# Kernel tuning notes

Measured on AMD Instinct MI355X. Metric: run time of the kernel, lower is better.

The kernel has to match this reference:

```python
import jax, jax.numpy as jnp
import numpy as np
from jax import lax

B, N = 1, 16384
HID = 128
ITERS = 32           # sphere_tracing_iters
SECANT_ITERS = 8     # root-finding refinement steps
THR = 1e-5           # root_finding_threshold
CLAMP = 0.1          # clamp_dist for sphere tracing steps
SN, SF = 16, 16      # near/far surface sample counts
SVR = 0.05           # surface_vol_range (meters)


def setup_inputs():
    key = jax.random.key(0)
    ks = jax.random.split(key, 10)
    cam_loc = jax.random.normal(ks[0], (B, 3)) * 0.1 + jnp.array([0.0, 0.0, 3.0])
    d = jax.random.normal(ks[1], (B, N, 3)) * 0.3 + jnp.array([0.0, 0.0, -1.0])
    ray_directions = d / jnp.linalg.norm(d, axis=-1, keepdims=True)
    near = 1.0 + 0.5 * jax.random.uniform(ks[2], (B, N))
    far = near + 1.0 + jax.random.uniform(ks[3], (B, N))
    body_bounds_intersections = jnp.stack([near, far], axis=-1)
    smpl_verts = jax.random.normal(ks[4], (B, 6890, 3)) * 0.5
    smpl_verts_cano = jax.random.normal(ks[5], (B, 6890, 3)) * 0.5
    sw = jax.random.uniform(ks[6], (B, 6890, 24))
    skinning_weights = sw / jnp.sum(sw, axis=-1, keepdims=True)
    bone_transforms = jnp.broadcast_to(jnp.eye(4), (B, 24, 4, 4)).copy()
    loc = jnp.zeros((B, 1, 3)); sc_factor = jnp.ones((B, 1, 3)); trans = jnp.zeros((B, 1, 3))
    coord_min = -1.2 * jnp.ones((B, 1, 3)); coord_max = 1.2 * jnp.ones((B, 1, 3)); center = jnp.zeros((B, 1, 3))
    W1 = jax.random.normal(ks[7], (3, HID)) / np.sqrt(3.0)
    W2 = jax.random.normal(ks[8], (HID, HID)) / np.sqrt(HID)
    W3 = jax.random.normal(ks[9], (HID, 1)) / np.sqrt(HID)
    b1 = jnp.zeros((HID,)); b2 = jnp.zeros((HID,)); b3 = jnp.zeros((1,))
    return dict(cam_loc=cam_loc, ray_directions=ray_directions,
                body_bounds_intersections=body_bounds_intersections, loc=loc,
                sc_factor=sc_factor, smpl_verts=smpl_verts, smpl_verts_cano=smpl_verts_cano,
                skinning_weights=skinning_weights, bone_transforms=bone_transforms, trans=trans,
                coord_min=coord_min, coord_max=coord_max, center=center,
                W1=W1, b1=b1, W2=W2, b2=b2, W3=W3, b3=b3)


def _forward(cam_loc, ray_directions, body_bounds_intersections, loc, sc_factor,
             smpl_verts, smpl_verts_cano, skinning_weights, bone_transforms, trans,
             coord_min, coord_max, center, W1, b1, W2, b2, W3, b3):
    cam = cam_loc[:, None, :]                       # [B,1,3]
    dirs = ray_directions                            # [B,N,3]
    near = body_bounds_intersections[..., 0]         # [B,N]
    far = body_bounds_intersections[..., 1]

    def to_cano(x):  # world -> normalized canonical coords
        x = (x - trans - loc) * sc_factor
        return (x - center) / ((coord_max - coord_min) * 0.5)

    def sdf_mlp(xn):
        h = jax.nn.softplus(xn @ W1 + b1)
        h = jax.nn.softplus(h @ W2 + b2)
        return (h @ W3 + b3)[..., 0]

    def sdf_at(t):  # t: [B,N] -> (sdf [B,N], pts_norm [B,N,3])
        xn = to_cano(cam + t[..., None] * dirs)
        return sdf_mlp(xn), xn

    # ---- sphere tracing (fixed ITERS, mask-based early exit) ----
    unf0 = near < far
    div0 = ~unf0
    pts0 = to_cano(cam + near[..., None] * dirs)

    def st_step(carry, _):
        acc, unf, div, pts = carry
        s, xn = sdf_at(acc)
        conv = unf
        pts = jnp.where(conv[..., None], xn, pts)
        sm = jnp.clip(s, -CLAMP, CLAMP)
        upd = unf & (jnp.abs(sm) > THR) & (jnp.abs(s) < 1e6)
        acc = jnp.where(upd, acc + sm, acc)
        div = jnp.where(upd, acc >= far, div)
        remove = (conv & (jnp.abs(s) <= THR)) | div
        unf = unf & ~remove
        return (acc, unf, div, pts), None

    (acc, unf, div, pts), _ = lax.scan(st_step, (near, unf0, div0, pts0), None, length=ITERS)

    # ---- secant root finding on ray depth ----
    t0 = jnp.clip(acc - CLAMP, near, far)
    t1 = jnp.clip(acc, near, far)
    f0, _ = sdf_at(t0)

    def sec_step(carry, _):
        t0, f0, t1 = carry
        f1, _ = sdf_at(t1)
        denom = f0 - f1
        denom = jnp.where(jnp.abs(denom) < 1e-9, 1e-9, denom)
        t2 = jnp.clip(t1 - f1 * (t1 - t0) / denom, near, far)
        return (t1, f1, t2), None

    (t0, f0, t1), _ = lax.scan(sec_step, (t0, f0, t1), None, length=SECANT_ITERS)
    f1, xn1 = sdf_at(t1)
    conv_opt = (jnp.abs(f1) <= THR) & (t1 >= near) & (t1 <= far)

    curr_start_points = xn1                                    # [B,N,3] normalized
    acc_start_dis = jnp.where(conv_opt, t1, near)              # [B,N]
    network_body_mask = conv_opt

    # per-ray forward transforms: LBS with mean skinning weights (skinning net surrogate)
    w_mean = jnp.mean(skinning_weights, axis=1)
    w_mean = w_mean / jnp.sum(w_mean, axis=-1, keepdims=True)  # [B,24]
    T = jnp.einsum('bj,bjkl->bkl', w_mean, bone_transforms)    # [B,4,4]
    S = SN + SF
    sampler_transforms = jnp.broadcast_to(T[:, None, None], (T.shape[0], t1.shape[1], S, 4, 4))

    # ---- ray sampler (eval mode: no perturbation) ----
    u_n = jnp.linspace(0.0, 1.0, SN)
    z_near = (t1 - SVR)[..., None] + u_n * (2.0 * SVR)         # [B,N,SN]
    u_f = jnp.linspace(0.0, 1.0, SF)
    z_far = near[..., None] + u_f * (far - near)[..., None]    # [B,N,SF]
    z_surf = jnp.sort(jnp.concatenate([z_near, z_far], axis=-1), axis=-1)
    u_a = jnp.linspace(0.0, 1.0, S)
    z_uni = near[..., None] + u_a * (far - near)[..., None]
    z = jnp.where(conv_opt[..., None], z_surf, z_uni)          # [B,N,S]
    sampler_pts = to_cano(cam[:, :, None, :] + z[..., None] * dirs[:, :, None, :])
    sampler_dists = z
    sampler_converge_mask = conv_opt

    return (curr_start_points, network_body_mask, acc_start_dis,
            sampler_pts, sampler_dists, sampler_transforms, sampler_converge_mask)


def reference(cam_loc, ray_directions, body_bounds_intersections, loc, sc_factor,
              smpl_verts, smpl_verts_cano, skinning_weights, bone_transforms, trans,
              coord_min, coord_max, center, W1, b1, W2, b2, W3, b3):
    return _forward(cam_loc, ray_directions, body_bounds_intersections, loc, sc_factor,
                    smpl_verts, smpl_verts_cano, skinning_weights, bone_transforms, trans,
                    coord_min, coord_max, center, W1, b1, W2, b2, W3, b3)
```

## Files before the change

kernel.cpp:

```cpp
#include <hip/hip_runtime.h>

typedef short sh8 __attribute__((ext_vector_type(8)));
typedef __bf16 bf8 __attribute__((ext_vector_type(8)));
typedef float f4 __attribute__((ext_vector_type(4)));
typedef unsigned int u4 __attribute__((ext_vector_type(4)));

#define DEV __device__ __forceinline__

DEV unsigned int fbits(float f){ union{float f;unsigned int u;}v; v.f=f; return v.u; }
DEV float bitsf(unsigned int u){ union{unsigned int u;float f;}v; v.u=u; return v.f; }
DEV float bf2f(unsigned short u) { return bitsf(((unsigned int)u) << 16); }
DEV unsigned short f2bf(float f) {
    unsigned int x = fbits(f);
    return (unsigned short)((x + 0x7fffu + ((x >> 16) & 1u)) >> 16);
}
DEV float sp_f(float x) {
    float ax = fabsf(x);
    float e  = exp2f(ax * -1.4426950408889634f);
    float u  = 1.0f + e;
    float c  = e - (u - 1.0f);
    float lg = log2f(u);
    return fmaxf(x, 0.0f) + fmaf(0.69314718055994531f, lg, c * (2.0f - u));
}

#define MFMA(a, b, c) __builtin_amdgcn_mfma_f32_16x16x32_bf16(__builtin_bit_cast(bf8, a), __builtin_bit_cast(bf8, b), c, 0, 0, 0)

__global__ void t_kernel(const float* __restrict__ sw,
                         const float* __restrict__ bt,
                         float* __restrict__ Tout, int V) {
    __shared__ float red[4 * 24];
    __shared__ float mm[24];
    float p[24];
#pragma unroll
    for (int j = 0; j < 24; j++) p[j] = 0.0f;
    for (int v = threadIdx.x; v < V; v += 256) {
        const float* row = sw + v * 24;
#pragma unroll
        for (int c4 = 0; c4 < 6; c4++) {
            f4 a = *(const f4*)(row + c4 * 4);
#pragma unroll
            for (int e = 0; e < 4; e++) p[c4 * 4 + e] += a[e];
        }
    }
#pragma unroll
    for (int j = 0; j < 24; j++) {
#pragma unroll
        for (int msk = 1; msk < 64; msk <<= 1) p[j] += __shfl_xor(p[j], msk);
    }
    int lane = threadIdx.x & 63, wid = threadIdx.x >> 6;
    if (lane == 0) {
#pragma unroll
        for (int j = 0; j < 24; j++) red[wid * 24 + j] = p[j];
    }
    __syncthreads();
    if (threadIdx.x < 24) {
        float s = red[threadIdx.x] + red[24 + threadIdx.x] + red[48 + threadIdx.x] + red[72 + threadIdx.x];
        mm[threadIdx.x] = s / (float)V;
    }
    __syncthreads();
    if (threadIdx.x < 16) {
        float tot = 0.0f;
#pragma unroll
        for (int j = 0; j < 24; j++) tot += mm[j];
        float a = 0.0f;
#pragma unroll
        for (int j = 0; j < 24; j++) a += (mm[j] / tot) * bt[j * 16 + threadIdx.x];
        Tout[threadIdx.x] = a;
    }
}

__global__ __launch_bounds__(256, 1) void main_kernel(
    const float* __restrict__ cam_loc, const float* __restrict__ dirs,
    const float* __restrict__ bbi,     const float* __restrict__ loc,
    const float* __restrict__ scf,     const float* __restrict__ trans,
    const float* __restrict__ cmin,    const float* __restrict__ cmax,
    const float* __restrict__ cent,    const float* __restrict__ W1,
    const float* __restrict__ b1,      const float* __restrict__ W2,
    const float* __restrict__ b2,      const float* __restrict__ W3,
    const float* __restrict__ b3,      const float* __restrict__ Tmat,
    float* __restrict__ out, int N) {

    __shared__ unsigned short wfrag[3 * 16384];
    __shared__ f4 w1p[16 * 9];
    __shared__ float b2s[128], w3s[128];

    const int tid = threadIdx.x;

    for (int i4 = tid; i4 < 4096; i4 += 256) {
        f4 v = *(const f4*)(W2 + i4 * 4);
        int k = (i4 * 4) >> 7;
        int n0 = (i4 * 4) & 127;
        int lanehalf = ((k >> 3) & 3) << 4;
        int fk = k >> 5;
        int j = k & 7;
#pragma unroll
        for (int e = 0; e < 4; e++) {
            int n = n0 + e;
            float w = v[e];
            unsigned short u0 = f2bf(w);   float g0 = bf2f(u0);
            float r1 = w - g0;             unsigned short u1 = f2bf(r1); float g1 = bf2f(u1);
            float r2 = r1 - g1;            unsigned short u2 = f2bf(r2);
            int off = ((n >> 4) * 4 + fk) * 512 + (lanehalf | (n & 15)) * 8 + j;
            wfrag[off]         = u0;
            wfrag[16384 + off] = u1;
            wfrag[32768 + off] = u2;
        }
    }
    if (tid < 128) {
        int k = tid, ks = k >> 5, uu = (k >> 3) & 3, j = k & 7;
        f4 w;
        w.x = W1[k]; w.y = W1[128 + k]; w.z = W1[256 + k]; w.w = b1[k];
        w1p[(ks * 4 + uu) * 9 + j] = w;
        b2s[k] = b2[k];
        w3s[k] = W3[k];
    }
    __syncthreads();

    const int lane = tid & 63;
    const int wv = tid >> 6;
    const int m = lane & 15, u = lane >> 4;
    const int rayBase = (blockIdx.x * 4 + wv) * 16;
    const int R = rayBase + m;

    const int O1 = 3 * N, O2 = 4 * N, O3 = 5 * N, O4 = 101 * N, O5 = 133 * N, O6 = 645 * N;

    float camx = cam_loc[0], camy = cam_loc[1], camz = cam_loc[2];
    float A[3], Bc[3];
#pragma unroll
    for (int c = 0; c < 3; c++) {
        float he = 0.5f * (cmax[c] - cmin[c]);
        float sc = scf[c];
        float off = (0.0f - trans[c] - loc[c]) * sc - cent[c];
        A[c] = sc / he; Bc[c] = off / he;
    }
    float dx = dirs[R * 3 + 0], dy = dirs[R * 3 + 1], dz = dirs[R * 3 + 2];
    float nearv = bbi[R * 2 + 0], farv = bbi[R * 2 + 1];

    float w3v[8], b2v[8];
#pragma unroll
    for (int nt = 0; nt < 8; nt++) { w3v[nt] = w3s[nt * 16 + m]; b2v[nt] = b2s[nt * 16 + m]; }
    float b3v = b3[0];

    const int lane16 = lane * 8;

    auto EVAL = [&](float t, float& sout) {
        float y0 = fmaf(t, dx, camx), y1 = fmaf(t, dy, camy), y2 = fmaf(t, dz, camz);
        float x0 = fmaf(y0, A[0], Bc[0]), x1 = fmaf(y1, A[1], Bc[1]), x2 = fmaf(y2, A[2], Bc[2]);
        f4 c[8];
#pragma unroll
        for (int f = 0; f < 8; f++) {
            float b = b2v[f];
            c[f] = (f4){b, b, b, b};
        }
#pragma unroll 1
        for (int ks = 0; ks < 4; ks++) {
            u4 a0w, a1w, a2w;
#pragma unroll
            for (int jp = 0; jp < 4; jp++) {
                f4 wA = w1p[(ks * 4 + u) * 9 + 2 * jp];
                f4 wB = w1p[(ks * 4 + u) * 9 + 2 * jp + 1];
                float hA = fmaf(x0, wA.x, fmaf(x1, wA.y, fmaf(x2, wA.z, wA.w)));
                float hB = fmaf(x0, wB.x, fmaf(x1, wB.y, fmaf(x2, wB.z, wB.w)));
                float sA = sp_f(hA), sB = sp_f(hB);
                unsigned short A0 = f2bf(sA); float fA0 = bf2f(A0);
                unsigned short B0 = f2bf(sB); float fB0 = bf2f(B0);
                float rA1 = sA - fA0, rB1 = sB - fB0;
                unsigned short A1 = f2bf(rA1); float fA1 = bf2f(A1);
                unsigned short B1 = f2bf(rB1); float fB1 = bf2f(B1);
                float rA2 = rA1 - fA1, rB2 = rB1 - fB1;
                unsigned short A2 = f2bf(rA2);
                unsigned short B2 = f2bf(rB2);
                a0w[jp] = (unsigned int)A0 | ((unsigned int)B0 << 16);
                a1w[jp] = (unsigned int)A1 | ((unsigned int)B1 << 16);
                a2w[jp] = (unsigned int)A2 | ((unsigned int)B2 << 16);
            }
            const int base = ks * 512 + lane16;
#pragma unroll
            for (int f = 0; f < 8; f++) {
                int fi = f * 2048 + base;
                sh8 b0 = *(const sh8*)&wfrag[fi];
                sh8 b1f = *(const sh8*)&wfrag[16384 + fi];
                sh8 b2f = *(const sh8*)&wfrag[32768 + fi];
                c[f] = MFMA(a0w, b0, c[f]);
                c[f] = MFMA(a1w, b0, c[f]);
                c[f] = MFMA(a2w, b0, c[f]);
                c[f] = MFMA(a0w, b1f, c[f]);
                c[f] = MFMA(a1w, b1f, c[f]);
                c[f] = MFMA(a0w, b2f, c[f]);
            }
        }
        float pr0 = 0.f, pr1 = 0.f, pr2 = 0.f, pr3 = 0.f;
#pragma unroll
        for (int f = 0; f < 8; f++) {
            float wv3 = w3v[f];
            pr0 = fmaf(sp_f(c[f].x), wv3, pr0);
            pr1 = fmaf(sp_f(c[f].y), wv3, pr1);
            pr2 = fmaf(sp_f(c[f].z), wv3, pr2);
            pr3 = fmaf(sp_f(c[f].w), wv3, pr3);
        }
#pragma unroll
        for (int msk = 1; msk < 16; msk <<= 1) {
            pr0 += __shfl_xor(pr0, msk); pr1 += __shfl_xor(pr1, msk);
            pr2 += __shfl_xor(pr2, msk); pr3 += __shfl_xor(pr3, msk);
        }
        pr0 += b3v; pr1 += b3v; pr2 += b3v; pr3 += b3v;
        int srcl = (m >> 2) << 4;
        float q0 = __shfl(pr0, srcl), q1 = __shfl(pr1, srcl);
        float q2 = __shfl(pr2, srcl), q3 = __shfl(pr3, srcl);
        float sa = (m & 1) ? q1 : q0, sb = (m & 1) ? q3 : q2;
        sout = (m & 2) ? sb : sa;
    };

    float acc = nearv;
    bool unf = nearv < farv;
    bool dv = !unf;
    float sv;
#pragma unroll 1
    for (int it = 0; it < 32; ++it) {
        if (!__any((int)unf)) break;
        EVAL(acc, sv);
        float smv = fminf(fmaxf(sv, -0.1f), 0.1f);
        bool convu = unf;
        bool upd = unf && (fabsf(smv) > 1e-5f) && (fabsf(sv) < 1000000.0f);
        if (upd) acc = acc + smv;
        dv = upd ? (acc >= farv) : dv;
        bool remove = (convu && (fabsf(sv) <= 1e-5f)) || dv;
        unf = unf && !remove;
    }

    float t0 = fminf(fmaxf(acc - 0.1f, nearv), farv);
    float t1 = fminf(fmaxf(acc, nearv), farv);
    float f0;
    EVAL(t0, f0);
    float f1 = 0.0f;
#pragma unroll 1
    for (int si = 0; si < 9; ++si) {
        float f1s;
        EVAL(t1, f1s);
        if (si == 8) { f1 = f1s; break; }
        float den = f0 - f1s;
        den = (fabsf(den) < 1e-9f) ? 1e-9f : den;
        float t2 = t1 - f1s * (t1 - t0) / den;
        t2 = fminf(fmaxf(t2, nearv), farv);
        t0 = t1; f0 = f1s; t1 = t2;
    }
    bool conv = (fabsf(f1) <= 1e-5f) && (t1 >= nearv) && (t1 <= farv);

    float xv0, xv1, xv2;
    {
        float y0 = fmaf(t1, dx, camx), y1 = fmaf(t1, dy, camy), y2 = fmaf(t1, dz, camz);
        xv0 = fmaf(y0, A[0], Bc[0]); xv1 = fmaf(y1, A[1], Bc[1]); xv2 = fmaf(y2, A[2], Bc[2]);
    }

    if (u == 0) {
        out[R * 3 + 0] = xv0;
        out[R * 3 + 1] = xv1;
        out[R * 3 + 2] = xv2;
        out[O1 + R] = conv ? 1.0f : 0.0f;
        out[O2 + R] = conv ? t1 : nearv;
        out[O6 + R] = conv ? 1.0f : 0.0f;
    }

    float zreg[8];
    if (conv) {
        float a0v = t1 - 0.05f, sa = 0.1f / 15.0f;
        float b0v = nearv, sb = (farv - nearv) / 15.0f;
        int ia = 0, ib = 0;
#pragma unroll
        for (int i = 0; i < 32; i++) {
            float va = fmaf((float)ia, sa, a0v);
            float vb = fmaf((float)ib, sb, b0v);
            bool ta = (ia < 16) && ((ib >= 16) || (va <= vb));
            float zv = ta ? va : vb;
            if (ta) ia++; else ib++;
            if ((i >> 3) == u) zreg[i & 7] = zv;
        }
    } else {
        float rng = farv - nearv;
#pragma unroll
        for (int q = 0; q < 8; q++) {
            int i = u * 8 + q;
            zreg[q] = fmaf((float)i * (1.0f / 31.0f), rng, nearv);
        }
    }

    {
        f4 d0, d1;
#pragma unroll
        for (int q = 0; q < 4; q++) { d0[q] = zreg[q]; d1[q] = zreg[4 + q]; }
        *(f4*)&out[O4 + R * 32 + u * 8] = d0;
        *(f4*)&out[O4 + R * 32 + u * 8 + 4] = d1;
    }

    {
        f4 pk[6];
#pragma unroll
        for (int q = 0; q < 8; q++) {
            float z = zreg[q];
            float y0 = fmaf(z, dx, camx), y1 = fmaf(z, dy, camy), y2 = fmaf(z, dz, camz);
            float v0 = fmaf(y0, A[0], Bc[0]);
            float v1 = fmaf(y1, A[1], Bc[1]);
            float v2 = fmaf(y2, A[2], Bc[2]);
#pragma unroll
            for (int c = 0; c < 3; c++) {
                int ee = q * 3 + c;
                float vv = (c == 0) ? v0 : ((c == 1) ? v1 : v2);
                pk[ee >> 2][ee & 3] = vv;
            }
        }
        int pbase = O3 + R * 96 + u * 24;
#pragma unroll
        for (int s6 = 0; s6 < 6; s6++) *(f4*)&out[pbase + s6 * 4] = pk[s6];
    }

    {
        f4 myrow = *(const f4*)&Tmat[(lane & 3) * 4];
        int base = O5 + rayBase * 512;
#pragma unroll
        for (int cc = 0; cc < 32; cc++) {
            int g = lane + 64 * cc;
            *(f4*)&out[base + g * 4] = myrow;
        }
    }
}

extern "C" void kernel_launch(void* const* d_in, const int* in_sizes, int n_in,
                              void* d_out, int out_size, void* d_ws, size_t ws_size,
                              hipStream_t stream) {
    (void)n_in; (void)out_size; (void)ws_size;
    const float* cam  = (const float*)d_in[0];
    const float* dirs = (const float*)d_in[1];
    const float* bbi  = (const float*)d_in[2];
    const float* loc  = (const float*)d_in[3];
    const float* scf  = (const float*)d_in[4];
    const float* sw   = (const float*)d_in[7];
    const float* bt   = (const float*)d_in[8];
    const float* trn  = (const float*)d_in[9];
    const float* cmn  = (const float*)d_in[10];
    const float* cmx  = (const float*)d_in[11];
    const float* cen  = (const float*)d_in[12];
    const float* W1   = (const float*)d_in[13];
    const float* b1   = (const float*)d_in[14];
    const float* W2   = (const float*)d_in[15];
    const float* b2   = (const float*)d_in[16];
    const float* W3   = (const float*)d_in[17];
    const float* b3   = (const float*)d_in[18];

    float* Tout = (float*)d_ws;
    int N = in_sizes[1] / 3;
    int V = in_sizes[7] / 24;

    hipLaunchKernelGGL(t_kernel, dim3(1), dim3(256), 0, stream, sw, bt, Tout, V);
    hipLaunchKernelGGL(main_kernel, dim3(N / 64), dim3(256), 0, stream,
                       cam, dirs, bbi, loc, scf, trn, cmn, cmx, cen,
                       W1, b1, W2, b2, W3, b3, Tout,
                       (float*)d_out, N);
}
```

Baseline: 377.5 us.

## Reorder MLP layer-2 loops: precompute all A fragments, accumulate per output tile

Computes all layer-1 softplus bf16 split fragments for every k-step up front, then iterates over output tiles, accumulating each tile across k-steps and applying layer-3 softplus/dot immediately. This replaces eight live accumulators with one, and lets each tile's softplus epilogue interleave with the next tile's MFMAs. The trade is that all A fragments (48 registers) stay live through the MFMA phase and the layer-1 loop is fully unrolled, which changes register pressure and occupancy.

Result: slower. 389.7 us (+3.2%).

```diff
diff --git a/kernel.cpp b/kernel.cpp
--- a/kernel.cpp
+++ b/kernel.cpp
@@ -146,15 +146,9 @@
     auto EVAL = [&](float t, float& sout) {
         float y0 = fmaf(t, dx, camx), y1 = fmaf(t, dy, camy), y2 = fmaf(t, dz, camz);
         float x0 = fmaf(y0, A[0], Bc[0]), x1 = fmaf(y1, A[1], Bc[1]), x2 = fmaf(y2, A[2], Bc[2]);
-        f4 c[8];
-#pragma unroll
-        for (int f = 0; f < 8; f++) {
-            float b = b2v[f];
-            c[f] = (f4){b, b, b, b};
-        }
-#pragma unroll 1
+        u4 a0w[4], a1w[4], a2w[4];
+#pragma unroll
         for (int ks = 0; ks < 4; ks++) {
-            u4 a0w, a1w, a2w;
 #pragma unroll
             for (int jp = 0; jp < 4; jp++) {
                 f4 wA = w1p[(ks * 4 + u) * 9 + 2 * jp];
@@ -170,33 +164,34 @@
                 float rA2 = rA1 - fA1, rB2 = rB1 - fB1;
                 unsigned short A2 = f2bf(rA2);
                 unsigned short B2 = f2bf(rB2);
-                a0w[jp] = (unsigned int)A0 | ((unsigned int)B0 << 16);
-                a1w[jp] = (unsigned int)A1 | ((unsigned int)B1 << 16);
-                a2w[jp] = (unsigned int)A2 | ((unsigned int)B2 << 16);
+                a0w[ks][jp] = (unsigned int)A0 | ((unsigned int)B0 << 16);
+                a1w[ks][jp] = (unsigned int)A1 | ((unsigned int)B1 << 16);
+                a2w[ks][jp] = (unsigned int)A2 | ((unsigned int)B2 << 16);
             }
-            const int base = ks * 512 + lane16;
-#pragma unroll
-            for (int f = 0; f < 8; f++) {
-                int fi = f * 2048 + base;
+        }
+        float pr0 = 0.f, pr1 = 0.f, pr2 = 0.f, pr3 = 0.f;
+#pragma unroll 2
+        for (int f = 0; f < 8; f++) {
+            float b = b2v[f];
+            f4 cf = (f4){b, b, b, b};
+#pragma unroll
+            for (int ks = 0; ks < 4; ks++) {
+                int fi = f * 2048 + ks * 512 + lane16;
                 sh8 b0 = *(const sh8*)&wfrag[fi];
                 sh8 b1f = *(const sh8*)&wfrag[16384 + fi];
                 sh8 b2f = *(const sh8*)&wfrag[32768 + fi];
-                c[f] = MFMA(a0w, b0, c[f]);
-                c[f] = MFMA(a1w, b0, c[f]);
-                c[f] = MFMA(a2w, b0, c[f]);
-                c[f] = MFMA(a0w, b1f, c[f]);
-                c[f] = MFMA(a1w, b1f, c[f]);
-                c[f] = MFMA(a0w, b2f, c[f]);
+                cf = MFMA(a0w[ks], b0, cf);
+                cf = MFMA(a1w[ks], b0, cf);
+                cf = MFMA(a2w[ks], b0, cf);
+                cf = MFMA(a0w[ks], b1f, cf);
+                cf = MFMA(a1w[ks], b1f, cf);
+                cf = MFMA(a0w[ks], b2f, cf);
             }
-        }
-        float pr0 = 0.f, pr1 = 0.f, pr2 = 0.f, pr3 = 0.f;
-#pragma unroll
-        for (int f = 0; f < 8; f++) {
             float wv3 = w3v[f];
-            pr0 = fmaf(sp_f(c[f].x), wv3, pr0);
-            pr1 = fmaf(sp_f(c[f].y), wv3, pr1);
-            pr2 = fmaf(sp_f(c[f].z), wv3, pr2);
-            pr3 = fmaf(sp_f(c[f].w), wv3, pr3);
+            pr0 = fmaf(sp_f(cf.x), wv3, pr0);
+            pr1 = fmaf(sp_f(cf.y), wv3, pr1);
+            pr2 = fmaf(sp_f(cf.z), wv3, pr2);
+            pr3 = fmaf(sp_f(cf.w), wv3, pr3);
         }
 #pragma unroll
         for (int msk = 1; msk < 16; msk <<= 1) {
```

## Split each ray group's MLP K-dimension across two waves with LDS reduction

Applied to the files above, without the earlier changes.

Doubles the block to 512 threads and pairs waves so each wave of a pair computes half of the hidden-layer K reduction for the same 16 rays. Partial accumulators and partial output sums are exchanged through shared memory with block-wide barriers, and the tail output writes are split between the two waves. The early exit when all rays have converged is removed, since a wave can no longer leave the loop on its own while its partner still needs it at the barriers. This aims to raise occupancy and cut per-wave serial MFMA latency, at the cost of extra syncthreads, LDS traffic and always running all iterations.

Result: slower. 428.6 us (+13.5%).

```diff
diff --git a/kernel.cpp b/kernel.cpp
--- a/kernel.cpp
+++ b/kernel.cpp
@@ -69,7 +69,7 @@
     }
 }
 
-__global__ __launch_bounds__(256, 1) void main_kernel(
+__global__ __launch_bounds__(512, 2) void main_kernel(
     const float* __restrict__ cam_loc, const float* __restrict__ dirs,
     const float* __restrict__ bbi,     const float* __restrict__ loc,
     const float* __restrict__ scf,     const float* __restrict__ trans,
@@ -81,12 +81,14 @@
     float* __restrict__ out, int N) {
 
     __shared__ unsigned short wfrag[3 * 16384];
+    __shared__ f4 red_c[4][2][4][64];
+    __shared__ float red_s[4][2][16];
     __shared__ f4 w1p[16 * 9];
     __shared__ float b2s[128], w3s[128];
 
     const int tid = threadIdx.x;
 
-    for (int i4 = tid; i4 < 4096; i4 += 256) {
+    for (int i4 = tid; i4 < 4096; i4 += 512) {
         f4 v = *(const f4*)(W2 + i4 * 4);
         int k = (i4 * 4) >> 7;
         int n0 = (i4 * 4) & 127;
@@ -118,8 +120,10 @@
 
     const int lane = tid & 63;
     const int wv = tid >> 6;
+    const int grp = wv >> 1;
+    const int half = wv & 1;
     const int m = lane & 15, u = lane >> 4;
-    const int rayBase = (blockIdx.x * 4 + wv) * 16;
+    const int rayBase = (blockIdx.x * 4 + grp) * 16;
     const int R = rayBase + m;
 
     const int O1 = 3 * N, O2 = 4 * N, O3 = 5 * N, O4 = 101 * N, O5 = 133 * N, O6 = 645 * N;
@@ -136,9 +140,12 @@
     float dx = dirs[R * 3 + 0], dy = dirs[R * 3 + 1], dz = dirs[R * 3 + 2];
     float nearv = bbi[R * 2 + 0], farv = bbi[R * 2 + 1];
 
-    float w3v[8], b2v[8];
-#pragma unroll
-    for (int nt = 0; nt < 8; nt++) { w3v[nt] = w3s[nt * 16 + m]; b2v[nt] = b2s[nt * 16 + m]; }
+    float w3q[4];
+#pragma unroll
+    for (int q = 0; q < 4; q++) w3q[q] = w3s[(half * 4 + q) * 16 + m];
+    float b2v[8];
+#pragma unroll
+    for (int f = 0; f < 8; f++) b2v[f] = half ? 0.0f : b2s[f * 16 + m];
     float b3v = b3[0];
 
     const int lane16 = lane * 8;
@@ -153,7 +160,8 @@
             c[f] = (f4){b, b, b, b};
         }
 #pragma unroll 1
-        for (int ks = 0; ks < 4; ks++) {
+        for (int ks2 = 0; ks2 < 2; ks2++) {
+            const int ks = half * 2 + ks2;
             u4 a0w, a1w, a2w;
 #pragma unroll
             for (int jp = 0; jp < 4; jp++) {
@@ -189,26 +197,35 @@
                 c[f] = MFMA(a0w, b2f, c[f]);
             }
         }
+#pragma unroll
+        for (int q = 0; q < 4; q++)
+            red_c[grp][half][q][lane] = c[(1 - half) * 4 + q];
+        __syncthreads();
         float pr0 = 0.f, pr1 = 0.f, pr2 = 0.f, pr3 = 0.f;
 #pragma unroll
-        for (int f = 0; f < 8; f++) {
-            float wv3 = w3v[f];
-            pr0 = fmaf(sp_f(c[f].x), wv3, pr0);
-            pr1 = fmaf(sp_f(c[f].y), wv3, pr1);
-            pr2 = fmaf(sp_f(c[f].z), wv3, pr2);
-            pr3 = fmaf(sp_f(c[f].w), wv3, pr3);
+        for (int q = 0; q < 4; q++) {
+            f4 cc = c[half * 4 + q] + red_c[grp][1 - half][q][lane];
+            float wv3 = w3q[q];
+            pr0 = fmaf(sp_f(cc.x), wv3, pr0);
+            pr1 = fmaf(sp_f(cc.y), wv3, pr1);
+            pr2 = fmaf(sp_f(cc.z), wv3, pr2);
+            pr3 = fmaf(sp_f(cc.w), wv3, pr3);
         }
 #pragma unroll
         for (int msk = 1; msk < 16; msk <<= 1) {
             pr0 += __shfl_xor(pr0, msk); pr1 += __shfl_xor(pr1, msk);
             pr2 += __shfl_xor(pr2, msk); pr3 += __shfl_xor(pr3, msk);
         }
-        pr0 += b3v; pr1 += b3v; pr2 += b3v; pr3 += b3v;
+        float prm = (m == 0) ? pr0 : (m == 1) ? pr1 : (m == 2) ? pr2 : pr3;
+        if (m < 4) red_s[grp][half][u * 4 + m] = prm;
+        __syncthreads();
+        float oth = red_s[grp][1 - half][m];
         int srcl = (m >> 2) << 4;
         float q0 = __shfl(pr0, srcl), q1 = __shfl(pr1, srcl);
         float q2 = __shfl(pr2, srcl), q3 = __shfl(pr3, srcl);
         float sa = (m & 1) ? q1 : q0, sb = (m & 1) ? q3 : q2;
-        sout = (m & 2) ? sb : sa;
+        float mine = (m & 2) ? sb : sa;
+        sout = (mine + oth) + b3v;
     };
 
     float acc = nearv;
@@ -217,7 +234,6 @@
     float sv;
 #pragma unroll 1
     for (int it = 0; it < 32; ++it) {
-        if (!__any((int)unf)) break;
         EVAL(acc, sv);
         float smv = fminf(fmaxf(sv, -0.1f), 0.1f);
         bool convu = unf;
@@ -252,7 +268,7 @@
         xv0 = fmaf(y0, A[0], Bc[0]); xv1 = fmaf(y1, A[1], Bc[1]); xv2 = fmaf(y2, A[2], Bc[2]);
     }
 
-    if (u == 0) {
+    if (u == 0 && half == 0) {
         out[R * 3 + 0] = xv0;
         out[R * 3 + 1] = xv1;
         out[R * 3 + 2] = xv2;
@@ -261,63 +277,63 @@
         out[O6 + R] = conv ? 1.0f : 0.0f;
     }
 
-    float zreg[8];
-    if (conv) {
-        float a0v = t1 - 0.05f, sa = 0.1f / 15.0f;
-        float b0v = nearv, sb = (farv - nearv) / 15.0f;
-        int ia = 0, ib = 0;
-#pragma unroll
-        for (int i = 0; i < 32; i++) {
-            float va = fmaf((float)ia, sa, a0v);
-            float vb = fmaf((float)ib, sb, b0v);
-            bool ta = (ia < 16) && ((ib >= 16) || (va <= vb));
-            float zv = ta ? va : vb;
-            if (ta) ia++; else ib++;
-            if ((i >> 3) == u) zreg[i & 7] = zv;
-        }
-    } else {
-        float rng = farv - nearv;
-#pragma unroll
-        for (int q = 0; q < 8; q++) {
-            int i = u * 8 + q;
-            zreg[q] = fmaf((float)i * (1.0f / 31.0f), rng, nearv);
-        }
-    }
-
-    {
-        f4 d0, d1;
-#pragma unroll
-        for (int q = 0; q < 4; q++) { d0[q] = zreg[q]; d1[q] = zreg[4 + q]; }
-        *(f4*)&out[O4 + R * 32 + u * 8] = d0;
-        *(f4*)&out[O4 + R * 32 + u * 8 + 4] = d1;
-    }
-
-    {
-        f4 pk[6];
-#pragma unroll
-        for (int q = 0; q < 8; q++) {
-            float z = zreg[q];
-            float y0 = fmaf(z, dx, camx), y1 = fmaf(z, dy, camy), y2 = fmaf(z, dz, camz);
-            float v0 = fmaf(y0, A[0], Bc[0]);
-            float v1 = fmaf(y1, A[1], Bc[1]);
-            float v2 = fmaf(y2, A[2], Bc[2]);
-#pragma unroll
-            for (int c = 0; c < 3; c++) {
-                int ee = q * 3 + c;
-                float vv = (c == 0) ? v0 : ((c == 1) ? v1 : v2);
-                pk[ee >> 2][ee & 3] = vv;
-            }
-        }
-        int pbase = O3 + R * 96 + u * 24;
-#pragma unroll
-        for (int s6 = 0; s6 < 6; s6++) *(f4*)&out[pbase + s6 * 4] = pk[s6];
+    if (half == 0) {
+        float zreg[8];
+        if (conv) {
+            float a0v = t1 - 0.05f, sa = 0.1f / 15.0f;
+            float b0v = nearv, sb = (farv - nearv) / 15.0f;
+            int ia = 0, ib = 0;
+#pragma unroll
+            for (int i = 0; i < 32; i++) {
+                float va = fmaf((float)ia, sa, a0v);
+                float vb = fmaf((float)ib, sb, b0v);
+                bool ta = (ia < 16) && ((ib >= 16) || (va <= vb));
+                float zv = ta ? va : vb;
+                if (ta) ia++; else ib++;
+                if ((i >> 3) == u) zreg[i & 7] = zv;
+            }
+        } else {
+            float rng = farv - nearv;
+#pragma unroll
+            for (int q = 0; q < 8; q++) {
+                int i = u * 8 + q;
+                zreg[q] = fmaf((float)i * (1.0f / 31.0f), rng, nearv);
+            }
+        }
+        {
+            f4 d0, d1;
+#pragma unroll
+            for (int q = 0; q < 4; q++) { d0[q] = zreg[q]; d1[q] = zreg[4 + q]; }
+            *(f4*)&out[O4 + R * 32 + u * 8] = d0;
+            *(f4*)&out[O4 + R * 32 + u * 8 + 4] = d1;
+        }
+        {
+            f4 pk[6];
+#pragma unroll
+            for (int q = 0; q < 8; q++) {
+                float z = zreg[q];
+                float y0 = fmaf(z, dx, camx), y1 = fmaf(z, dy, camy), y2 = fmaf(z, dz, camz);
+                float v0 = fmaf(y0, A[0], Bc[0]);
+                float v1 = fmaf(y1, A[1], Bc[1]);
+                float v2 = fmaf(y2, A[2], Bc[2]);
+#pragma unroll
+                for (int c = 0; c < 3; c++) {
+                    int ee = q * 3 + c;
+                    float vv = (c == 0) ? v0 : ((c == 1) ? v1 : v2);
+                    pk[ee >> 2][ee & 3] = vv;
+                }
+            }
+            int pbase = O3 + R * 96 + u * 24;
+#pragma unroll
+            for (int s6 = 0; s6 < 6; s6++) *(f4*)&out[pbase + s6 * 4] = pk[s6];
+        }
     }
 
     {
         f4 myrow = *(const f4*)&Tmat[(lane & 3) * 4];
         int base = O5 + rayBase * 512;
-#pragma unroll
-        for (int cc = 0; cc < 32; cc++) {
+        int cb = half ? 8 : 0, ce = half ? 32 : 8;
+        for (int cc = cb; cc < ce; cc++) {
             int g = lane + 64 * cc;
             *(f4*)&out[base + g * 4] = myrow;
         }
@@ -351,7 +367,7 @@
     int V = in_sizes[7] / 24;
 
     hipLaunchKernelGGL(t_kernel, dim3(1), dim3(256), 0, stream, sw, bt, Tout, V);
-    hipLaunchKernelGGL(main_kernel, dim3(N / 64), dim3(256), 0, stream,
+    hipLaunchKernelGGL(main_kernel, dim3(N / 64), dim3(512), 0, stream,
                        cam, dirs, bbi, loc, scf, trn, cmn, cmx, cen,
                        W1, b1, W2, b2, W3, b3, Tout,
                        (float*)d_out, N);
```
